# Optimization experiments

Measured on AMD Instinct MI355X. Metric: run time of the kernel, lower is better.

The kernel has to match this reference:

```python
import math
import jax, jax.numpy as jnp
import numpy as np

UNITS = 256
D_IN = 256
BATCH = 65536
STRENGTH = 0.5
PERIOD = 25.0
LAMBDA_SLOW = 0.1
JITTER = 0.05
H_INERTIA = 0.9
REST_BASELINE = 1.0


def setup_inputs() -> dict:
    key = jax.random.key(0)
    k1, k2, k3, k4, k5, k6 = jax.random.split(key, 6)
    glorot = math.sqrt(2.0 / (D_IN + UNITS))
    return {
        "inputs": jax.random.normal(k1, (BATCH, D_IN), dtype=jnp.float32),
        "prev_h": jax.random.normal(k2, (BATCH, UNITS), dtype=jnp.float32),
        "prev_G": jax.random.normal(k3, (BATCH, UNITS), dtype=jnp.float32),
        "prev_phase": jax.random.normal(k4, (BATCH, 1), dtype=jnp.float32),
        "w_in": jax.random.normal(k5, (D_IN, UNITS), dtype=jnp.float32) * glorot,
        "w_rec": jax.random.normal(k6, (UNITS, UNITS), dtype=jnp.float32) * (1.0 / math.sqrt(UNITS)),
        "bias": jnp.zeros((UNITS,), dtype=jnp.float32),
    }


def reference(inputs, prev_h, prev_G, prev_phase, w_in, w_rec, bias):
    half = UNITS // 2
    # roll-like swap of the two halves of the hidden state
    raw_signal = jnp.concatenate([prev_h[:, half:], prev_h[:, :half]], axis=1)
    # slow exponential-moving-average field
    new_G = (1.0 - LAMBDA_SLOW) * prev_G + LAMBDA_SLOW * raw_signal
    mean = jnp.mean(new_G, axis=-1, keepdims=True)
    std = jnp.std(new_G, axis=-1, keepdims=True)  # population std, matches tf.math.reduce_std
    G_norm = (new_G - mean) / (std + 1e-6)
    new_phase = prev_phase + 2.0 * math.pi / PERIOD
    oscillator = jnp.sin(new_phase)
    bias_signal = jnp.mean(raw_signal, axis=-1, keepdims=True) - 0.1
    combined_signal = oscillator + JITTER * bias_signal
    field_effect = REST_BASELINE + STRENGTH * combined_signal * jnp.tanh(G_norm)
    z = (inputs @ w_in + prev_h @ w_rec + bias) * field_effect
    h = H_INERTIA * prev_h + (1.0 - H_INERTIA) * jax.nn.elu(z)
    h = jnp.clip(h, -20.0, 20.0)
    return (h, new_G, new_phase)
```

## Files before the change

kernel.cpp:

```cpp
#include <hip/hip_runtime.h>

typedef unsigned short ushort_t;
typedef short v8s __attribute__((ext_vector_type(8)));
typedef float v4f __attribute__((ext_vector_type(4)));

#define BATCH    65536
#define UNITS    256
#define M_TILE   64
#define KSTEPS   16
#define BCHUNK   10240
#define T_STRIDE 264
#define LDS_HB   0
#define LDS_GT   33792
#define LDS_SC   67584
#define LDS_TOT  69376

__device__ __forceinline__ float b2f(ushort_t u) {
    union { unsigned int i; float f; } v; v.i = ((unsigned int)u) << 16; return v.f;
}
__device__ __forceinline__ ushort_t f2b(float f) {
    union { float f; unsigned int i; } v; v.f = f;
    unsigned int r = (v.i + 0x7fffu + ((v.i >> 16) & 1u)) >> 16;
    return (ushort_t)r;
}

__global__ void pack_w(const float* __restrict__ w_in,
                       const float* __restrict__ w_rec,
                       ushort_t* __restrict__ Wp) {
    int gid = blockIdx.x * 256 + threadIdx.x;
    int k = gid >> 8, n = gid & 255;
    float v = (k < 256) ? w_in[k * 256 + n] : w_rec[(k - 256) * 256 + n];
    Wp[(size_t)(k >> 5) * BCHUNK + n * 40 + (k & 31)] = f2b(v);
}

__global__ __launch_bounds__(256, 2)
void fused_cell(const float* __restrict__ inputs,
                const float* __restrict__ prev_h,
                const float* __restrict__ prev_G,
                const float* __restrict__ prev_phase,
                const ushort_t* __restrict__ Wp,
                const float* __restrict__ bias,
                float* __restrict__ out) {
    __shared__ __align__(16) char smem[LDS_TOT];
    short* Hb     = (short*)(smem + LDS_HB);
    short* Gt     = (short*)(smem + LDS_GT);
    float* r_mean = (float*)(smem + LDS_SC);
    float* r_rstd = r_mean + 64;
    float* r_comb = r_rstd + 64;
    float* bias_f = r_comb + 64;

    const int tid  = threadIdx.x;
    const int l    = tid & 63;
    const int w    = tid >> 6;
    const int row0 = blockIdx.x * M_TILE;

    float* outH = out;
    float* outG = out + (size_t)BATCH * UNITS;
    float* outP = out + (size_t)2 * BATCH * UNITS;

    bias_f[tid] = bias[tid];

    for (int rr = 0; rr < 16; ++rr) {
        int lr = w * 16 + rr;
        int gr = row0 + lr;
        int c0 = l * 4;
        int pc = (c0 + 128) & 255;
        float4 hp = *(const float4*)(prev_h + (size_t)gr * UNITS + pc);
        float4 gp = *(const float4*)(prev_G + (size_t)gr * UNITS + c0);
        float4 ng;
        ng.x = 0.9f * gp.x + 0.1f * hp.x;
        ng.y = 0.9f * gp.y + 0.1f * hp.y;
        ng.z = 0.9f * gp.z + 0.1f * hp.z;
        ng.w = 0.9f * gp.w + 0.1f * hp.w;
        float s1 = ng.x + ng.y + ng.z + ng.w;
        float s2 = ng.x*ng.x + ng.y*ng.y + ng.z*ng.z + ng.w*ng.w;
        float sh = hp.x + hp.y + hp.z + hp.w;
        *(float4*)(outG + (size_t)gr * UNITS + c0) = ng;
        ushort4 gq; gq.x = f2b(ng.x); gq.y = f2b(ng.y); gq.z = f2b(ng.z); gq.w = f2b(ng.w);
        *(ushort4*)(Gt + lr * T_STRIDE + c0) = gq;
        ushort4 hq; hq.x = f2b(hp.x); hq.y = f2b(hp.y); hq.z = f2b(hp.z); hq.w = f2b(hp.w);
        *(ushort4*)(Hb + lr * T_STRIDE + pc) = hq;
        #pragma unroll
        for (int off = 32; off > 0; off >>= 1) {
            s1 += __shfl_xor(s1, off, 64);
            s2 += __shfl_xor(s2, off, 64);
            sh += __shfl_xor(sh, off, 64);
        }
        if (l == 0) {
            float mean = s1 * (1.f / 256.f);
            float var  = s2 * (1.f / 256.f) - mean * mean;
            float rstd = 1.f / (sqrtf(fmaxf(var, 0.f)) + 1e-6f);
            float np   = prev_phase[gr] + 0.2513274122871834591f;
            outP[gr] = np;
            float comb = sinf(np) + 0.05f * (sh * (1.f / 256.f) - 0.1f);
            r_mean[lr] = mean; r_rstd[lr] = rstd; r_comb[lr] = comb;
        }
    }

    __syncthreads();

    const int n16 = l & 15;
    const int q   = l >> 4;
    v4f acc[16];
    const v4f z4 = {0.f, 0.f, 0.f, 0.f};
    #pragma unroll
    for (int t = 0; t < 16; ++t) acc[t] = z4;

    const int arow = w * 16 + n16;
    const float* ainp = inputs + (size_t)(row0 + arow) * UNITS + q * 8;
    const short* hbp  = Hb + arow * T_STRIDE + q * 8;
    const short* bp   = (const short*)Wp + n16 * 40 + q * 8;

    #pragma unroll 2
    for (int s = 0; s < KSTEPS; ++s) {
        v8s a;
        if (s < 8) {
            float4 f0 = *(const float4*)(ainp + s * 32);
            float4 f1 = *(const float4*)(ainp + s * 32 + 4);
            a[0] = (short)f2b(f0.x); a[1] = (short)f2b(f0.y);
            a[2] = (short)f2b(f0.z); a[3] = (short)f2b(f0.w);
            a[4] = (short)f2b(f1.x); a[5] = (short)f2b(f1.y);
            a[6] = (short)f2b(f1.z); a[7] = (short)f2b(f1.w);
        } else {
            a = *(const v8s*)(hbp + (s - 8) * 32);
        }
        const short* bs = bp + s * BCHUNK;
        #pragma unroll
        for (int t = 0; t < 16; ++t) {
            v8s b = *(const v8s*)(bs + t * 640);
            acc[t] = __builtin_amdgcn_mfma_f32_16x16x32_bf16(a, b, acc[t], 0, 0, 0);
        }
    }

    #pragma unroll
    for (int t = 0; t < 16; ++t) {
        int c = t * 16 + n16;
        float bz = bias_f[c];
        #pragma unroll
        for (int r = 0; r < 4; ++r) {
            int lr = w * 16 + q * 4 + r;
            int gr = row0 + lr;
            float gval = b2f((ushort_t)Gt[lr * T_STRIDE + c]);
            float gn = (gval - r_mean[lr]) * r_rstd[lr];
            float e2 = __expf(2.f * gn);
            float th = 1.f - 2.f / (e2 + 1.f);
            float field = 1.f + 0.5f * r_comb[lr] * th;
            float z = (acc[t][r] + bz) * field;
            float el = (z > 0.f) ? z : (__expf(z) - 1.f);
            float h = 0.9f * b2f((ushort_t)Hb[lr * T_STRIDE + c]) + 0.1f * el;
            h = fminf(fmaxf(h, -20.f), 20.f);
            outH[(size_t)gr * UNITS + c] = h;
        }
    }
}

extern "C" void kernel_launch(void* const* d_in, const int* in_sizes, int n_in,
                              void* d_out, int out_size, void* d_ws, size_t ws_size,
                              hipStream_t stream) {
    const float* inputs     = (const float*)d_in[0];
    const float* prev_h     = (const float*)d_in[1];
    const float* prev_G     = (const float*)d_in[2];
    const float* prev_phase = (const float*)d_in[3];
    const float* w_in       = (const float*)d_in[4];
    const float* w_rec      = (const float*)d_in[5];
    const float* bias       = (const float*)d_in[6];
    float* out    = (float*)d_out;
    ushort_t* Wp  = (ushort_t*)d_ws;

    pack_w<<<512, 256, 0, stream>>>(w_in, w_rec, Wp);
    fused_cell<<<BATCH / M_TILE, 256, 0, stream>>>(inputs, prev_h, prev_G,
                                                   prev_phase, Wp, bias, out);
}
```

Before: 345.3 us.

## Double-buffer weight chunks in LDS via async loads and drop H/G tiles

Weight K-chunks are now streamed into a double-buffered LDS region with global_load_lds, and the next chunk's load is issued while the current chunk's MFMAs run. The next step's A operand is prefetched from global memory, and the recurrent half now reads prev_h directly instead of a bf16 LDS copy. The epilogue rereads the G and h values from global memory, which removes the bf16 H/G LDS tiles. The smaller LDS footprint allows occupancy 3. In exchange the kernel adds a barrier per K step and extra global rereads, and it relies on just-written outG being visible to other threads in the block.

```diff
diff --git a/kernel.cpp b/kernel.cpp
--- a/kernel.cpp
+++ b/kernel.cpp
@@ -9,11 +9,9 @@
 #define M_TILE   64
 #define KSTEPS   16
 #define BCHUNK   10240
-#define T_STRIDE 264
-#define LDS_HB   0
-#define LDS_GT   33792
-#define LDS_SC   67584
-#define LDS_TOT  69376
+#define BCHUNK_B 20480
+#define LDS_SC   40960
+#define LDS_TOT  42752
 
 __device__ __forceinline__ float b2f(ushort_t u) {
     union { unsigned int i; float f; } v; v.i = ((unsigned int)u) << 16; return v.f;
@@ -22,6 +20,19 @@
     union { float f; unsigned int i; } v; v.f = f;
     unsigned int r = (v.i + 0x7fffu + ((v.i >> 16) & 1u)) >> 16;
     return (ushort_t)r;
+}
+__device__ __forceinline__ v8s cvt8(float4 f0, float4 f1) {
+    v8s a;
+    a[0] = (short)f2b(f0.x); a[1] = (short)f2b(f0.y);
+    a[2] = (short)f2b(f0.z); a[3] = (short)f2b(f0.w);
+    a[4] = (short)f2b(f1.x); a[5] = (short)f2b(f1.y);
+    a[6] = (short)f2b(f1.z); a[7] = (short)f2b(f1.w);
+    return a;
+}
+__device__ __forceinline__ void cp16_async(char* lds, const char* g) {
+    __builtin_amdgcn_global_load_lds(
+        (const __attribute__((address_space(1))) unsigned int*)g,
+        (__attribute__((address_space(3))) unsigned int*)lds, 16, 0, 0);
 }
 
 __global__ void pack_w(const float* __restrict__ w_in,
@@ -33,7 +44,7 @@
     Wp[(size_t)(k >> 5) * BCHUNK + n * 40 + (k & 31)] = f2b(v);
 }
 
-__global__ __launch_bounds__(256, 2)
+__global__ __launch_bounds__(256, 3)
 void fused_cell(const float* __restrict__ inputs,
                 const float* __restrict__ prev_h,
                 const float* __restrict__ prev_G,
@@ -42,8 +53,7 @@
                 const float* __restrict__ bias,
                 float* __restrict__ out) {
     __shared__ __align__(16) char smem[LDS_TOT];
-    short* Hb     = (short*)(smem + LDS_HB);
-    short* Gt     = (short*)(smem + LDS_GT);
+    short* Bbuf   = (short*)(smem);
     float* r_mean = (float*)(smem + LDS_SC);
     float* r_rstd = r_mean + 64;
     float* r_comb = r_rstd + 64;
@@ -57,6 +67,15 @@
     float* outH = out;
     float* outG = out + (size_t)BATCH * UNITS;
     float* outP = out + (size_t)2 * BATCH * UNITS;
+
+    {
+        const char* g = (const char*)Wp;
+        #pragma unroll
+        for (int j = 0; j < 5; ++j) {
+            int off = j * 4096 + tid * 16;
+            cp16_async(smem + off, g + off);
+        }
+    }
 
     bias_f[tid] = bias[tid];
 
@@ -76,10 +95,6 @@
         float s2 = ng.x*ng.x + ng.y*ng.y + ng.z*ng.z + ng.w*ng.w;
         float sh = hp.x + hp.y + hp.z + hp.w;
         *(float4*)(outG + (size_t)gr * UNITS + c0) = ng;
-        ushort4 gq; gq.x = f2b(ng.x); gq.y = f2b(ng.y); gq.z = f2b(ng.z); gq.w = f2b(ng.w);
-        *(ushort4*)(Gt + lr * T_STRIDE + c0) = gq;
-        ushort4 hq; hq.x = f2b(hp.x); hq.y = f2b(hp.y); hq.z = f2b(hp.z); hq.w = f2b(hp.w);
-        *(ushort4*)(Hb + lr * T_STRIDE + pc) = hq;
         #pragma unroll
         for (int off = 32; off > 0; off >>= 1) {
             s1 += __shfl_xor(s1, off, 64);
@@ -108,28 +123,33 @@
 
     const int arow = w * 16 + n16;
     const float* ainp = inputs + (size_t)(row0 + arow) * UNITS + q * 8;
-    const short* hbp  = Hb + arow * T_STRIDE + q * 8;
-    const short* bp   = (const short*)Wp + n16 * 40 + q * 8;
+    const float* ahp  = prev_h + (size_t)(row0 + arow) * UNITS + q * 8;
 
-    #pragma unroll 2
+    v8s a_cur = cvt8(*(const float4*)(ainp), *(const float4*)(ainp + 4));
+
     for (int s = 0; s < KSTEPS; ++s) {
-        v8s a;
-        if (s < 8) {
-            float4 f0 = *(const float4*)(ainp + s * 32);
-            float4 f1 = *(const float4*)(ainp + s * 32 + 4);
-            a[0] = (short)f2b(f0.x); a[1] = (short)f2b(f0.y);
-            a[2] = (short)f2b(f0.z); a[3] = (short)f2b(f0.w);
-            a[4] = (short)f2b(f1.x); a[5] = (short)f2b(f1.y);
-            a[6] = (short)f2b(f1.z); a[7] = (short)f2b(f1.w);
-        } else {
-            a = *(const v8s*)(hbp + (s - 8) * 32);
+        float4 f0n, f1n;
+        if (s + 1 < KSTEPS) {
+            const char* g = (const char*)(Wp + (size_t)(s + 1) * BCHUNK);
+            char* lp = smem + ((s + 1) & 1) * BCHUNK_B;
+            #pragma unroll
+            for (int j = 0; j < 5; ++j) {
+                int off = j * 4096 + tid * 16;
+                cp16_async(lp + off, g + off);
+            }
+            int sn = s + 1;
+            const float* ap = (sn < 8) ? (ainp + sn * 32) : (ahp + (sn - 8) * 32);
+            f0n = *(const float4*)(ap);
+            f1n = *(const float4*)(ap + 4);
         }
-        const short* bs = bp + s * BCHUNK;
+        const short* bb = Bbuf + (s & 1) * BCHUNK + n16 * 40 + q * 8;
         #pragma unroll
         for (int t = 0; t < 16; ++t) {
-            v8s b = *(const v8s*)(bs + t * 640);
-            acc[t] = __builtin_amdgcn_mfma_f32_16x16x32_bf16(a, b, acc[t], 0, 0, 0);
+            v8s b = *(const v8s*)(bb + t * 640);
+            acc[t] = __builtin_amdgcn_mfma_f32_16x16x32_bf16(a_cur, b, acc[t], 0, 0, 0);
         }
+        __syncthreads();
+        if (s + 1 < KSTEPS) a_cur = cvt8(f0n, f1n);
     }
 
     #pragma unroll
@@ -140,14 +160,14 @@
         for (int r = 0; r < 4; ++r) {
             int lr = w * 16 + q * 4 + r;
             int gr = row0 + lr;
-            float gval = b2f((ushort_t)Gt[lr * T_STRIDE + c]);
+            float gval = outG[(size_t)gr * UNITS + c];
             float gn = (gval - r_mean[lr]) * r_rstd[lr];
             float e2 = __expf(2.f * gn);
             float th = 1.f - 2.f / (e2 + 1.f);
             float field = 1.f + 0.5f * r_comb[lr] * th;
             float z = (acc[t][r] + bz) * field;
             float el = (z > 0.f) ? z : (__expf(z) - 1.f);
-            float h = 0.9f * b2f((ushort_t)Hb[lr * T_STRIDE + c]) + 0.1f * el;
+            float h = 0.9f * prev_h[(size_t)gr * UNITS + c] + 0.1f * el;
             h = fminf(fmaxf(h, -20.f), 20.f);
             outH[(size_t)gr * UNITS + c] = h;
         }
```

After: 383.1 us. +10.9%, slower.
